# Performance work log

Hardware: AMD Instinct MI355X
Metric: run time of the kernel (lower is better)

The kernel has to match this reference:

```python
import jax, jax.numpy as jnp
import numpy as np

NUM_CLASSES = 100  # matches labels fill_max
N, D = 131072, 512


def setup_inputs() -> dict:
    key = jax.random.key(0)
    kf, kl = jax.random.split(key)
    features = jax.random.normal(kf, (N, D), dtype=jnp.float32)
    labels = jax.random.randint(kl, (N,), 0, NUM_CLASSES, dtype=jnp.int64)
    return {"features": features, "labels": labels}


def reference(features, labels):
    # Per-class segment reductions: counts, sum of features, sum of squared norms.
    # trace(cov_c) = (sum_i ||x_i||^2 - n_c * ||mu_c||^2) / (n_c - 1)
    ones = jnp.ones((features.shape[0],), dtype=features.dtype)
    counts = jax.ops.segment_sum(ones, labels, num_segments=NUM_CLASSES)          # [C]
    sums = jax.ops.segment_sum(features, labels, num_segments=NUM_CLASSES)        # [C, D]
    sq = jax.ops.segment_sum(jnp.sum(features * features, axis=1), labels,
                             num_segments=NUM_CLASSES)                            # [C]
    safe_n = jnp.maximum(counts, 1.0)
    mu = sums / safe_n[:, None]                                                   # [C, D]
    ssd = sq - counts * jnp.sum(mu * mu, axis=1)                                  # sum sq deviations
    trace = ssd / jnp.maximum(counts - 1.0, 1.0)                                  # [C]
    valid = counts >= 2.0
    valid_count = jnp.sum(valid.astype(features.dtype))
    total = jnp.sum(jnp.where(valid, trace, 0.0))
    loss = jnp.where(valid_count > 0, total / jnp.maximum(valid_count, 1.0), 0.0)
    return loss
```

## Files before the change

kernel.cpp:

```cpp
#include <hip/hip_runtime.h>

#define NCLASS 100
#define DDIM   512
#define NROWS  131072

#define CHUNK    2048
#define NCHUNK   (NROWS / CHUNK)
#define NSPLIT   8
#define AWAVES   8
#define WSLOTS   (NSPLIT * AWAVES)
#define SPAN     (CHUNK / WSLOTS)
#define ATHREADS 512
#define STHREADS 1024

__global__ __launch_bounds__(STHREADS) void icv_sort_kernel(
    const int* __restrict__ labels,
    int* __restrict__ rows_g,
    int* __restrict__ off_g,
    int* __restrict__ cnt_p,
    int* __restrict__ span_g,
    int* __restrict__ sync_cnt)
{
    __shared__ int s_cnt[NCLASS];
    __shared__ int s_off[NCLASS + 1];
    __shared__ int s_pos[NCLASS];
    __shared__ int s_scan[128];
    __shared__ int s_rows[CHUNK];

    const int tid   = threadIdx.x;
    const int chunk = blockIdx.x;
    const int row0  = chunk * CHUNK;

    if (tid < NCLASS) s_cnt[tid] = 0;
    if (chunk == 0 && tid == 0) *sync_cnt = 0;
    __syncthreads();

    const int lab0 = labels[row0 + tid];
    const int lab1 = labels[row0 + STHREADS + tid];
    atomicAdd(&s_cnt[lab0], 1);
    atomicAdd(&s_cnt[lab1], 1);
    __syncthreads();

    if (tid < 128) s_scan[tid] = (tid < NCLASS) ? s_cnt[tid] : 0;
    __syncthreads();
    #pragma unroll
    for (int d = 1; d < 128; d <<= 1) {
        int v = 0;
        if (tid < 128) { v = s_scan[tid]; if (tid >= d) v += s_scan[tid - d]; }
        __syncthreads();
        if (tid < 128) s_scan[tid] = v;
        __syncthreads();
    }
    if (tid < NCLASS) { const int e = s_scan[tid] - s_cnt[tid]; s_off[tid] = e; s_pos[tid] = e; }
    if (tid == NCLASS) s_off[NCLASS] = CHUNK;
    __syncthreads();

    { const int p0 = atomicAdd(&s_pos[lab0], 1); s_rows[p0] = row0 + tid; }
    { const int p1 = atomicAdd(&s_pos[lab1], 1); s_rows[p1] = row0 + STHREADS + tid; }

    if (tid < WSLOTS) {
        int cf = NCLASS, ce = NCLASS;
        for (int c = 0; c < NCLASS; ++c) {
            int ow = s_off[c] / SPAN; if (ow > WSLOTS - 1) ow = WSLOTS - 1;
            if (ow == tid && cf == NCLASS) cf = c;
            if (ow > tid) { ce = c; break; }
        }
        if (cf > ce) cf = ce;
        span_g[(chunk * WSLOTS + tid) * 2 + 0] = cf;
        span_g[(chunk * WSLOTS + tid) * 2 + 1] = ce;
    }
    __syncthreads();

    rows_g[chunk * CHUNK + tid]            = s_rows[tid];
    rows_g[chunk * CHUNK + STHREADS + tid] = s_rows[STHREADS + tid];
    if (tid < NCLASS) {
        off_g[chunk * (NCLASS + 1) + tid] = s_off[tid];
        cnt_p[chunk * NCLASS + tid]       = s_cnt[tid];
    }
    if (tid == NCLASS) off_g[chunk * (NCLASS + 1) + NCLASS] = CHUNK;
}

__global__ __launch_bounds__(ATHREADS, 4) void icv_accum_kernel(
    const float* __restrict__ feat,
    const int*   __restrict__ rows_g,
    const int*   __restrict__ off_g,
    const int*   __restrict__ span_g,
    float*       __restrict__ sums_p,
    float*       __restrict__ sq_p)
{
    __shared__ int s_rows[CHUNK];
    __shared__ int s_off[NCLASS + 1];

    const int tid   = threadIdx.x;
    const int wave  = tid >> 6;
    const int lane  = tid & 63;
    const int b     = blockIdx.x;
    const int chunk = b >> 3;
    const int split = b & 7;

    #pragma unroll
    for (int k = 0; k < CHUNK / ATHREADS; ++k)
        s_rows[k * ATHREADS + tid] = rows_g[chunk * CHUNK + k * ATHREADS + tid];
    if (tid < NCLASS + 1) s_off[tid] = off_g[chunk * (NCLASS + 1) + tid];
    __syncthreads();

    const int ws = split * AWAVES + wave;
    const int cf = span_g[(chunk * WSLOTS + ws) * 2 + 0];
    const int ce = span_g[(chunk * WSLOTS + ws) * 2 + 1];
    const int i0 = s_off[cf];
    const int i1 = s_off[ce];

    const float4* f4 = (const float4*)feat;

    int    c    = cf;
    int    cend = (c < ce) ? s_off[c + 1] : (CHUNK + 1);
    float4 accA = make_float4(0.f, 0.f, 0.f, 0.f);
    float4 accB = make_float4(0.f, 0.f, 0.f, 0.f);
    float  sq   = 0.f;

#define LOADA(idx) f4[(size_t)s_rows[(idx)] * (DDIM / 4) + lane]
#define LOADB(idx) f4[(size_t)s_rows[(idx)] * (DDIM / 4) + 64 + lane]

#define FLUSH() do {                                                          \
        float s_ = sq;                                                        \
        s_ += __shfl_xor(s_, 32, 64); s_ += __shfl_xor(s_, 16, 64);           \
        s_ += __shfl_xor(s_,  8, 64); s_ += __shfl_xor(s_,  4, 64);           \
        s_ += __shfl_xor(s_,  2, 64); s_ += __shfl_xor(s_,  1, 64);           \
        float4* dst_ = (float4*)(sums_p                                       \
            + ((size_t)(chunk * NCLASS + c) * DDIM));                         \
        dst_[lane]      = accA;                                               \
        dst_[64 + lane] = accB;                                               \
        if (lane == 0) sq_p[chunk * NCLASS + c] = s_;                         \
        accA = make_float4(0.f, 0.f, 0.f, 0.f);                               \
        accB = make_float4(0.f, 0.f, 0.f, 0.f);                               \
        sq = 0.f;                                                             \
        ++c;                                                                  \
        cend = (c < ce) ? s_off[c + 1] : (CHUNK + 1);                         \
    } while (0)

#define STEP(K, RA, RB) {                                                     \
        const int i_ = ib + (K);                                              \
        if (i_ < i1) {                                                        \
            while (i_ >= cend) FLUSH();                                       \
            const float4 a_ = RA;                                             \
            const float4 b_ = RB;                                             \
            const int ip_ = i_ + 4;                                           \
            if (ip_ < i1) { RA = LOADA(ip_); RB = LOADB(ip_); }               \
            accA.x += a_.x; accA.y += a_.y; accA.z += a_.z; accA.w += a_.w;   \
            accB.x += b_.x; accB.y += b_.y; accB.z += b_.z; accB.w += b_.w;   \
            sq = fmaf(a_.x, a_.x, fmaf(a_.y, a_.y,                            \
                 fmaf(a_.z, a_.z, fmaf(a_.w, a_.w, sq))));                    \
            sq = fmaf(b_.x, b_.x, fmaf(b_.y, b_.y,                            \
                 fmaf(b_.z, b_.z, fmaf(b_.w, b_.w, sq))));                    \
        }                                                                     \
    }

    float4 r0a = make_float4(0.f, 0.f, 0.f, 0.f), r0b = r0a;
    float4 r1a = r0a, r1b = r0a, r2a = r0a, r2b = r0a, r3a = r0a, r3b = r0a;
    if (i0 + 0 < i1) { r0a = LOADA(i0 + 0); r0b = LOADB(i0 + 0); }
    if (i0 + 1 < i1) { r1a = LOADA(i0 + 1); r1b = LOADB(i0 + 1); }
    if (i0 + 2 < i1) { r2a = LOADA(i0 + 2); r2b = LOADB(i0 + 2); }
    if (i0 + 3 < i1) { r3a = LOADA(i0 + 3); r3b = LOADB(i0 + 3); }

    for (int ib = i0; ib < i1; ib += 4) {
        STEP(0, r0a, r0b)
        STEP(1, r1a, r1b)
        STEP(2, r2a, r2b)
        STEP(3, r3a, r3b)
    }
    while (c < ce) FLUSH();
#undef STEP
#undef FLUSH
#undef LOADA
#undef LOADB
}

__global__ __launch_bounds__(512) void icv_reduce_kernel(
    const float* __restrict__ sums_p,
    const float* __restrict__ sq_p,
    const int*   __restrict__ cnt_p,
    float*       __restrict__ cls_out,
    int*         __restrict__ sync_cnt,
    float*       __restrict__ out)
{
    __shared__ float red[3][8];
    __shared__ float fin[2][8];
    __shared__ int   s_last;

    const int c    = blockIdx.x;
    const int t    = threadIdx.x;
    const int wave = t >> 6;
    const int lane = t & 63;

    float s = 0.f;
    const float* p = sums_p + (size_t)c * DDIM + t;
    #pragma unroll 8
    for (int ch = 0; ch < NCHUNK; ++ch)
        s += p[(size_t)ch * (NCLASS * DDIM)];

    float v1 = s * s;
    float v2 = (t < NCHUNK) ? sq_p[t * NCLASS + c] : 0.f;
    float v3 = (t < NCHUNK) ? (float)cnt_p[t * NCLASS + c] : 0.f;
    #pragma unroll
    for (int off = 32; off > 0; off >>= 1) {
        v1 += __shfl_xor(v1, off, 64);
        v2 += __shfl_xor(v2, off, 64);
        v3 += __shfl_xor(v3, off, 64);
    }
    if (lane == 0) { red[0][wave] = v1; red[1][wave] = v2; red[2][wave] = v3; }
    __syncthreads();

    if (t == 0) {
        float n2 = 0.f, sq = 0.f, n = 0.f;
        #pragma unroll
        for (int w = 0; w < 8; ++w) { n2 += red[0][w]; sq += red[1][w]; n += red[2][w]; }
        const float safe  = fmaxf(n, 1.f);
        const float ssd   = sq - n2 / safe;
        const float trace = ssd / fmaxf(n - 1.f, 1.f);
        const bool  valid = (n >= 2.f);
        cls_out[c * 2 + 0] = valid ? trace : 0.f;
        cls_out[c * 2 + 1] = valid ? 1.f : 0.f;
        __threadfence();
        const int done = atomicAdd(sync_cnt, 1);
        s_last = (done == NCLASS - 1) ? 1 : 0;
    }
    __syncthreads();

    if (s_last) {
        __threadfence();
        float tv = 0.f, vv = 0.f;
        if (t < NCLASS) {
            const volatile float* cv = (const volatile float*)cls_out;
            tv = cv[t * 2 + 0];
            vv = cv[t * 2 + 1];
        }
        #pragma unroll
        for (int off = 32; off > 0; off >>= 1) {
            tv += __shfl_xor(tv, off, 64);
            vv += __shfl_xor(vv, off, 64);
        }
        if (lane == 0) { fin[0][wave] = tv; fin[1][wave] = vv; }
        __syncthreads();
        if (t == 0) {
            float tot = 0.f, vc = 0.f;
            #pragma unroll
            for (int w = 0; w < 8; ++w) { tot += fin[0][w]; vc += fin[1][w]; }
            out[0] = (vc > 0.f) ? (tot / fmaxf(vc, 1.f)) : 0.f;
        }
    }
}

extern "C" void kernel_launch(void* const* d_in, const int* in_sizes, int n_in,
                              void* d_out, int out_size, void* d_ws, size_t ws_size,
                              hipStream_t stream) {
    const float* feat   = (const float*)d_in[0];
    const int*   labels = (const int*)d_in[1];
    float* out = (float*)d_out;

    float* sums_p  = (float*)d_ws;
    float* sq_p    = sums_p + (size_t)NCHUNK * NCLASS * DDIM;
    int*   cnt_p   = (int*)(sq_p + NCHUNK * NCLASS);
    int*   rows_g  = cnt_p + NCHUNK * NCLASS;
    int*   off_g   = rows_g + NCHUNK * CHUNK;
    int*   span_g  = off_g + NCHUNK * (NCLASS + 1);
    float* cls_out = (float*)(span_g + NCHUNK * WSLOTS * 2);
    int*   sync_cnt= (int*)(cls_out + NCLASS * 2);

    icv_sort_kernel<<<dim3(NCHUNK), STHREADS, 0, stream>>>(
        labels, rows_g, off_g, cnt_p, span_g, sync_cnt);
    icv_accum_kernel<<<dim3(NCHUNK * NSPLIT), ATHREADS, 0, stream>>>(
        feat, rows_g, off_g, span_g, sums_p, sq_p);
    icv_reduce_kernel<<<dim3(NCLASS), 512, 0, stream>>>(
        sums_p, sq_p, cnt_p, cls_out, sync_cnt, out);
}
```

Measured before the change: 73.99 us.

## Split reduce kernel into four blocks per class and rebalance class-to-wave spans

The final reduce kernel now launches four 128-thread blocks per class instead of one 512-thread block. Each block sums one quarter of the feature dimension and adds its partial squared norm into a per-class accumulator with a float atomic. The final trace computation moves into the last-finishing block. Separately, the sort kernel assigns each class to a wave slot by the class's midpoint rather than its start offset, to balance the accumulate work. This exposes more blocks for the memory-bound partial-sum reduction, at the cost of extra atomics and nondeterministic float summation order.

```diff
diff --git a/kernel.cpp b/kernel.cpp
--- a/kernel.cpp
+++ b/kernel.cpp
@@ -13,13 +13,18 @@
 #define ATHREADS 512
 #define STHREADS 1024
 
+__device__ __forceinline__ void gAtomicAddF(float* p, float v) {
+    unsafeAtomicAdd(p, v);
+}
+
 __global__ __launch_bounds__(STHREADS) void icv_sort_kernel(
     const int* __restrict__ labels,
-    int* __restrict__ rows_g,
-    int* __restrict__ off_g,
-    int* __restrict__ cnt_p,
-    int* __restrict__ span_g,
-    int* __restrict__ sync_cnt)
+    int*   __restrict__ rows_g,
+    int*   __restrict__ off_g,
+    int*   __restrict__ cnt_p,
+    int*   __restrict__ span_g,
+    float* __restrict__ cls_norm2,
+    int*   __restrict__ sync_cnt)
 {
     __shared__ int s_cnt[NCLASS];
     __shared__ int s_off[NCLASS + 1];
@@ -32,7 +37,10 @@
     const int row0  = chunk * CHUNK;
 
     if (tid < NCLASS) s_cnt[tid] = 0;
-    if (chunk == 0 && tid == 0) *sync_cnt = 0;
+    if (chunk == 0) {
+        if (tid < NCLASS) cls_norm2[tid] = 0.f;
+        if (tid == 0) *sync_cnt = 0;
+    }
     __syncthreads();
 
     const int lab0 = labels[row0 + tid];
@@ -61,7 +69,8 @@
     if (tid < WSLOTS) {
         int cf = NCLASS, ce = NCLASS;
         for (int c = 0; c < NCLASS; ++c) {
-            int ow = s_off[c] / SPAN; if (ow > WSLOTS - 1) ow = WSLOTS - 1;
+            const int mid = (s_off[c] + s_off[c + 1]) >> 1;
+            int ow = mid / SPAN; if (ow > WSLOTS - 1) ow = WSLOTS - 1;
             if (ow == tid && cf == NCLASS) cf = c;
             if (ow > tid) { ce = c; break; }
         }
@@ -175,54 +184,54 @@
 #undef LOADB
 }
 
-__global__ __launch_bounds__(512) void icv_reduce_kernel(
+__global__ __launch_bounds__(128) void icv_reduce_kernel(
     const float* __restrict__ sums_p,
     const float* __restrict__ sq_p,
     const int*   __restrict__ cnt_p,
-    float*       __restrict__ cls_out,
+    float*       __restrict__ cls_norm2,
+    float*       __restrict__ cls_sq,
+    float*       __restrict__ cls_n,
     int*         __restrict__ sync_cnt,
     float*       __restrict__ out)
 {
-    __shared__ float red[3][8];
-    __shared__ float fin[2][8];
+    __shared__ float sred[2];
+    __shared__ float fin[2][2];
     __shared__ int   s_last;
 
-    const int c    = blockIdx.x;
-    const int t    = threadIdx.x;
-    const int wave = t >> 6;
-    const int lane = t & 63;
+    const int c = blockIdx.x >> 2;
+    const int q = blockIdx.x & 3;
+    const int t = threadIdx.x;
 
     float s = 0.f;
-    const float* p = sums_p + (size_t)c * DDIM + t;
-    #pragma unroll 8
+    const float* p = sums_p + (size_t)c * DDIM + (q * 128 + t);
+    #pragma unroll 16
     for (int ch = 0; ch < NCHUNK; ++ch)
         s += p[(size_t)ch * (NCLASS * DDIM)];
 
-    float v1 = s * s;
-    float v2 = (t < NCHUNK) ? sq_p[t * NCLASS + c] : 0.f;
-    float v3 = (t < NCHUNK) ? (float)cnt_p[t * NCLASS + c] : 0.f;
-    #pragma unroll
-    for (int off = 32; off > 0; off >>= 1) {
-        v1 += __shfl_xor(v1, off, 64);
-        v2 += __shfl_xor(v2, off, 64);
-        v3 += __shfl_xor(v3, off, 64);
-    }
-    if (lane == 0) { red[0][wave] = v1; red[1][wave] = v2; red[2][wave] = v3; }
+    float v = s * s;
+    v += __shfl_xor(v, 32, 64); v += __shfl_xor(v, 16, 64);
+    v += __shfl_xor(v,  8, 64); v += __shfl_xor(v,  4, 64);
+    v += __shfl_xor(v,  2, 64); v += __shfl_xor(v,  1, 64);
+    if ((t & 63) == 0) sred[t >> 6] = v;
+
+    if (t < 64 && q == 0) {
+        float v2 = (t < NCHUNK) ? sq_p[t * NCLASS + c] : 0.f;
+        float v3 = (t < NCHUNK) ? (float)cnt_p[t * NCLASS + c] : 0.f;
+        v2 += __shfl_xor(v2, 32, 64); v3 += __shfl_xor(v3, 32, 64);
+        v2 += __shfl_xor(v2, 16, 64); v3 += __shfl_xor(v3, 16, 64);
+        v2 += __shfl_xor(v2,  8, 64); v3 += __shfl_xor(v3,  8, 64);
+        v2 += __shfl_xor(v2,  4, 64); v3 += __shfl_xor(v3,  4, 64);
+        v2 += __shfl_xor(v2,  2, 64); v3 += __shfl_xor(v3,  2, 64);
+        v2 += __shfl_xor(v2,  1, 64); v3 += __shfl_xor(v3,  1, 64);
+        if (t == 0) { cls_sq[c] = v2; cls_n[c] = v3; }
+    }
     __syncthreads();
 
     if (t == 0) {
-        float n2 = 0.f, sq = 0.f, n = 0.f;
-        #pragma unroll
-        for (int w = 0; w < 8; ++w) { n2 += red[0][w]; sq += red[1][w]; n += red[2][w]; }
-        const float safe  = fmaxf(n, 1.f);
-        const float ssd   = sq - n2 / safe;
-        const float trace = ssd / fmaxf(n - 1.f, 1.f);
-        const bool  valid = (n >= 2.f);
-        cls_out[c * 2 + 0] = valid ? trace : 0.f;
-        cls_out[c * 2 + 1] = valid ? 1.f : 0.f;
+        gAtomicAddF(&cls_norm2[c], sred[0] + sred[1]);
         __threadfence();
         const int done = atomicAdd(sync_cnt, 1);
-        s_last = (done == NCLASS - 1) ? 1 : 0;
+        s_last = (done == NCLASS * 4 - 1) ? 1 : 0;
     }
     __syncthreads();
 
@@ -230,22 +239,31 @@
         __threadfence();
         float tv = 0.f, vv = 0.f;
         if (t < NCLASS) {
-            const volatile float* cv = (const volatile float*)cls_out;
-            tv = cv[t * 2 + 0];
-            vv = cv[t * 2 + 1];
+            const volatile float* vn = cls_norm2;
+            const volatile float* vq = cls_sq;
+            const volatile float* vc = cls_n;
+            const float n    = vc[t];
+            const float n2   = vn[t];
+            const float sqv  = vq[t];
+            const float safe = fmaxf(n, 1.f);
+            const float ssd  = sqv - n2 / safe;
+            const float tr   = ssd / fmaxf(n - 1.f, 1.f);
+            const bool  valid = (n >= 2.f);
+            tv = valid ? tr : 0.f;
+            vv = valid ? 1.f : 0.f;
         }
-        #pragma unroll
-        for (int off = 32; off > 0; off >>= 1) {
-            tv += __shfl_xor(tv, off, 64);
-            vv += __shfl_xor(vv, off, 64);
-        }
-        if (lane == 0) { fin[0][wave] = tv; fin[1][wave] = vv; }
+        tv += __shfl_xor(tv, 32, 64); vv += __shfl_xor(vv, 32, 64);
+        tv += __shfl_xor(tv, 16, 64); vv += __shfl_xor(vv, 16, 64);
+        tv += __shfl_xor(tv,  8, 64); vv += __shfl_xor(vv,  8, 64);
+        tv += __shfl_xor(tv,  4, 64); vv += __shfl_xor(vv,  4, 64);
+        tv += __shfl_xor(tv,  2, 64); vv += __shfl_xor(vv,  2, 64);
+        tv += __shfl_xor(tv,  1, 64); vv += __shfl_xor(vv,  1, 64);
+        if ((t & 63) == 0) { fin[0][t >> 6] = tv; fin[1][t >> 6] = vv; }
         __syncthreads();
         if (t == 0) {
-            float tot = 0.f, vc = 0.f;
-            #pragma unroll
-            for (int w = 0; w < 8; ++w) { tot += fin[0][w]; vc += fin[1][w]; }
-            out[0] = (vc > 0.f) ? (tot / fmaxf(vc, 1.f)) : 0.f;
+            const float tot = fin[0][0] + fin[0][1];
+            const float vcn = fin[1][0] + fin[1][1];
+            out[0] = (vcn > 0.f) ? (tot / fmaxf(vcn, 1.f)) : 0.f;
         }
     }
 }
@@ -257,19 +275,21 @@
     const int*   labels = (const int*)d_in[1];
     float* out = (float*)d_out;
 
-    float* sums_p  = (float*)d_ws;
-    float* sq_p    = sums_p + (size_t)NCHUNK * NCLASS * DDIM;
-    int*   cnt_p   = (int*)(sq_p + NCHUNK * NCLASS);
-    int*   rows_g  = cnt_p + NCHUNK * NCLASS;
-    int*   off_g   = rows_g + NCHUNK * CHUNK;
-    int*   span_g  = off_g + NCHUNK * (NCLASS + 1);
-    float* cls_out = (float*)(span_g + NCHUNK * WSLOTS * 2);
-    int*   sync_cnt= (int*)(cls_out + NCLASS * 2);
+    float* sums_p    = (float*)d_ws;
+    float* sq_p      = sums_p + (size_t)NCHUNK * NCLASS * DDIM;
+    int*   cnt_p     = (int*)(sq_p + NCHUNK * NCLASS);
+    int*   rows_g    = cnt_p + NCHUNK * NCLASS;
+    int*   off_g     = rows_g + NCHUNK * CHUNK;
+    int*   span_g    = off_g + NCHUNK * (NCLASS + 1);
+    float* cls_norm2 = (float*)(span_g + NCHUNK * WSLOTS * 2);
+    float* cls_sq    = cls_norm2 + NCLASS;
+    float* cls_n     = cls_sq + NCLASS;
+    int*   sync_cnt  = (int*)(cls_n + NCLASS);
 
     icv_sort_kernel<<<dim3(NCHUNK), STHREADS, 0, stream>>>(
-        labels, rows_g, off_g, cnt_p, span_g, sync_cnt);
+        labels, rows_g, off_g, cnt_p, span_g, cls_norm2, sync_cnt);
     icv_accum_kernel<<<dim3(NCHUNK * NSPLIT), ATHREADS, 0, stream>>>(
         feat, rows_g, off_g, span_g, sums_p, sq_p);
-    icv_reduce_kernel<<<dim3(NCLASS), 512, 0, stream>>>(
-        sums_p, sq_p, cnt_p, cls_out, sync_cnt, out);
-}
+    icv_reduce_kernel<<<dim3(NCLASS * 4), 128, 0, stream>>>(
+        sums_p, sq_p, cnt_p, cls_norm2, cls_sq, cls_n, sync_cnt, out);
+}
```

After: 80.71 us. +9.1%, slower.
